# Performance work log

Measured on AMD Instinct MI355X. Metric: run time of the kernel, lower is better.

The kernel has to match this reference:

```python
import jax, jax.numpy as jnp
import numpy as np

N, K, DIM = 65536, 32, 64


def setup_inputs() -> dict:
    key = jax.random.key(0)
    k1, k2, k3, k4 = jax.random.split(key, 4)
    x = jax.random.normal(k1, (N, DIM), jnp.float32)
    log_pi = jax.random.normal(k2, (K, 1), jnp.float32)
    mu = jax.random.normal(k3, (K, DIM), jnp.float32)
    log_sigma_ = jax.random.normal(k4, (K, DIM, DIM), jnp.float32) / 100.0
    return {"x": x, "log_pi": log_pi, "mu": mu, "log_sigma_": log_sigma_}


def reference(x, log_pi, mu, log_sigma_):
    k, d = mu.shape
    # Faithful to torch: softmax over the size-1 last axis of (K,1) -> all ones.
    pi = jax.nn.softmax(log_pi, axis=-1)  # (K, 1)
    # scale_tril construction: strict lower triangle kept, diagonal -> exp(diag) + 1e-3
    diag = jnp.exp(jnp.diagonal(log_sigma_, axis1=-2, axis2=-1)) + 1e-3  # (K, d)
    L = jnp.tril(log_sigma_, -1) + jnp.eye(d, dtype=x.dtype) * diag[:, None, :]  # (K, d, d)
    # batched MVN log_prob via triangular solve
    diff = x[:, None, :] - mu[None, :, :]            # (N, K, d)
    b = jnp.transpose(diff, (1, 2, 0))               # (K, d, N)
    z = jax.scipy.linalg.solve_triangular(L, b, lower=True)  # (K, d, N)
    maha = jnp.sum(z * z, axis=1)                    # (K, N)
    logdet = jnp.sum(jnp.log(diag), axis=-1)         # (K,)
    logp = -0.5 * (maha + d * jnp.log(2.0 * jnp.pi)) - logdet[:, None]  # (K, N)
    p = jnp.exp(logp).T                              # (N, K)
    return jnp.log(jnp.matmul(p, pi).squeeze())      # (N,)
```

## Files before the change

### kernel.cpp

```cpp
#include <hip/hip_runtime.h>

#define KK 32
#define DD 64
#define NB 65536
#define PAD 68
#define FRAGS 6
#define SLOT (FRAGS * 64)
#define MREF 103.0f
#define L2E 1.4426950408889634f

typedef __attribute__((ext_vector_type(8))) short bf16x8;
typedef __attribute__((ext_vector_type(4))) float f32x4;
typedef __attribute__((ext_vector_type(16))) float f32x16;

__device__ inline short f2bf(float f) {
  uint32_t u = __builtin_bit_cast(uint32_t, f);
  uint32_t r = (u + 0x7fffu + ((u >> 16) & 1u)) >> 16;
  return (short)(r & 0xffffu);
}
__device__ inline uint4 pack8(const short* v) {
  uint4 u;
  u.x = (uint32_t)(unsigned short)v[0] | ((uint32_t)(unsigned short)v[1] << 16);
  u.y = (uint32_t)(unsigned short)v[2] | ((uint32_t)(unsigned short)v[3] << 16);
  u.z = (uint32_t)(unsigned short)v[4] | ((uint32_t)(unsigned short)v[5] << 16);
  u.w = (uint32_t)(unsigned short)v[6] | ((uint32_t)(unsigned short)v[7] << 16);
  return u;
}

__global__ __launch_bounds__(256) void md_prep(const float* __restrict__ ls,
                                               const float* __restrict__ mu,
                                               uint4* __restrict__ Bp,
                                               float* __restrict__ Cc,
                                               float* __restrict__ Kcl2) {
  __shared__ float Ls[DD * DD];
  __shared__ float Ys[DD * PAD];
  __shared__ float invdL[DD];
  __shared__ float muL[DD];
  const int k = blockIdx.x, t = threadIdx.x;
  const int j = t >> 2, sub = t & 3;
  const float* __restrict__ lsk = ls + (size_t)k * DD * DD;

#pragma unroll
  for (int it = 0; it < 4; ++it) {
    const int o = (it * 256 + t) * 4;
    *(float4*)&Ls[o] = *(const float4*)&lsk[o];
  }
  if (t < DD) muL[t] = mu[k * DD + t];
  __syncthreads();
  if (t < DD) invdL[t] = 1.0f / (expf(Ls[t * DD + t]) + 1e-3f);
  __syncthreads();

  const float invdj = invdL[j];
  float z[16];
#pragma unroll
  for (int mi = 0; mi < 16; ++mi) z[mi] = 0.f;
#pragma unroll
  for (int i = 0; i < DD; ++i) {
    float p = 0.f;
#pragma unroll
    for (int mi = 0; mi < 16; ++mi) {
      if (4 * mi < i) {
        const int m = 4 * mi + sub;
        p = fmaf(Ls[i * DD + m], (m < i) ? z[mi] : 0.f, p);
      }
    }
    p += __shfl_xor(p, 1, 64);
    p += __shfl_xor(p, 2, 64);
    const float zi = (i == j) ? invdj : -p * invdL[i];
    if (sub == (i & 3)) z[i >> 2] = zi;
  }
#pragma unroll
  for (int mi = 0; mi < 16; ++mi) Ys[(4 * mi + sub) * PAD + j] = z[mi];
  __syncthreads();

  {
    float p = 0.f;
#pragma unroll
    for (int mi = 0; mi < 16; ++mi) {
      const int m = 4 * mi + sub;
      p = fmaf(Ys[j * PAD + m], muL[m], p);
    }
    p += __shfl_xor(p, 1, 64);
    p += __shfl_xor(p, 2, 64);
    if (sub == 0) Cc[k * DD + j] = p;
  }

  if (t < DD) {
    float r = -logf(invdL[t]);
#pragma unroll
    for (int off = 32; off > 0; off >>= 1) r += __shfl_down(r, off, 64);
    if (t == 0)
      Kcl2[k] = (MREF - 0.5f * (64.0f * 1.83787706640934534f) - r) * L2E;
  }

  if (t < DD) {
    const int r32 = t & 31, h = t >> 5;
    uint4* slot = Bp + (size_t)k * SLOT;
#pragma unroll
    for (int it = 0; it < 2; ++it) {
#pragma unroll
      for (int kt = 0; kt < 4; ++kt) {
        if (it == 0 && kt >= 2) continue;
        const int i = it * 32 + r32;
        short hh[8];
#pragma unroll
        for (int jj = 0; jj < 8; ++jj) {
          const int m = kt * 16 + h * 8 + jj;
          const float v = Ys[i * PAD + m] - ((i == m) ? 1.0f : 0.0f);
          hh[jj] = f2bf(v);
        }
        const int fi = (it == 0) ? kt : (2 + kt);
        slot[fi * 64 + t] = pack8(hh);
      }
    }
  }
}

__global__ __launch_bounds__(256, 2) void md_main(const float* __restrict__ x,
                                                  const uint4* __restrict__ Bp,
                                                  const float* __restrict__ Cc,
                                                  const float* __restrict__ Kcl2,
                                                  float* __restrict__ out) {
  __shared__ float CcL[KK * DD];
  __shared__ float sOut[2 * 128];
  const int tid = threadIdx.x, lane = tid & 63, w = tid >> 6;
  const int sg = w & 1, kg = w >> 1;
  const int sblk = blockIdx.x;
  const int base = sblk * 128 + sg * 64;
  const int k0 = kg * 16;
  const int c32 = lane & 31, h = lane >> 5;

  bf16x8 Xb[2][4];
#pragma unroll
  for (int st = 0; st < 2; ++st) {
#pragma unroll
    for (int kt = 0; kt < 4; ++kt) {
      const float* src = x + (size_t)(base + st * 32 + c32) * DD + kt * 16 + h * 8;
      const float4 v0 = *(const float4*)src;
      const float4 v1 = *(const float4*)(src + 4);
      const float f[8] = {v0.x, v0.y, v0.z, v0.w, v1.x, v1.y, v1.z, v1.w};
      bf16x8 hb;
#pragma unroll
      for (int jj = 0; jj < 8; ++jj) hb[jj] = f2bf(f[jj]);
      Xb[st][kt] = hb;
    }
  }

  f32x16 xg[2][2];
#pragma unroll
  for (int it = 0; it < 2; ++it)
#pragma unroll
    for (int st = 0; st < 2; ++st)
#pragma unroll
      for (int g = 0; g < 4; ++g) {
        const f32x4 v = *(const f32x4*)&x[(size_t)(base + st * 32 + c32) * DD +
                                          it * 32 + g * 8 + 4 * h];
        xg[it][st][4 * g + 0] = v[0];
        xg[it][st][4 * g + 1] = v[1];
        xg[it][st][4 * g + 2] = v[2];
        xg[it][st][4 * g + 3] = v[3];
      }

#pragma unroll
  for (int it = 0; it < 8; ++it)
    CcL[it * 256 + tid] = Cc[it * 256 + tid];
  __syncthreads();

  float run_s[2] = {0.f, 0.f};

#pragma unroll
  for (int ci = 0; ci < 16; ++ci) {
    const int kabs = k0 + ci;
    const float kc = Kcl2[kabs];
    const uint4* __restrict__ buf = Bp + (size_t)kabs * SLOT;

    f32x4 cv[2][4];
#pragma unroll
    for (int it = 0; it < 2; ++it)
#pragma unroll
      for (int g = 0; g < 4; ++g)
        cv[it][g] = *(const f32x4*)&CcL[kabs * DD + it * 32 + g * 8 + 4 * h];

    const bf16x8 A0 = *(const bf16x8*)&buf[0 * 64 + lane];
    const bf16x8 A1 = *(const bf16x8*)&buf[1 * 64 + lane];
    const bf16x8 A2 = *(const bf16x8*)&buf[2 * 64 + lane];
    const bf16x8 A3 = *(const bf16x8*)&buf[3 * 64 + lane];
    const bf16x8 A4 = *(const bf16x8*)&buf[4 * 64 + lane];
    const bf16x8 A5 = *(const bf16x8*)&buf[5 * 64 + lane];

#pragma unroll
    for (int st = 0; st < 2; ++st) {
      f32x16 acc;
#pragma unroll
      for (int it = 0; it < 2; ++it) {
        f32x16 z;
#pragma unroll
        for (int g = 0; g < 4; ++g) {
#pragma unroll
          for (int r = 0; r < 4; ++r)
            z[4 * g + r] = xg[it][st][4 * g + r] - cv[it][g][r];
        }
        if (it == 0) {
          z = __builtin_amdgcn_mfma_f32_32x32x16_bf16(A0, Xb[st][0], z, 0, 0, 0);
          z = __builtin_amdgcn_mfma_f32_32x32x16_bf16(A1, Xb[st][1], z, 0, 0, 0);
          acc = z * z;
        } else {
          z = __builtin_amdgcn_mfma_f32_32x32x16_bf16(A2, Xb[st][0], z, 0, 0, 0);
          z = __builtin_amdgcn_mfma_f32_32x32x16_bf16(A3, Xb[st][1], z, 0, 0, 0);
          z = __builtin_amdgcn_mfma_f32_32x32x16_bf16(A4, Xb[st][2], z, 0, 0, 0);
          z = __builtin_amdgcn_mfma_f32_32x32x16_bf16(A5, Xb[st][3], z, 0, 0, 0);
          acc += z * z;
        }
      }
      const float t0 = (acc[0] + acc[1]) + (acc[2] + acc[3]);
      const float t1 = (acc[4] + acc[5]) + (acc[6] + acc[7]);
      const float t2 = (acc[8] + acc[9]) + (acc[10] + acc[11]);
      const float t3 = (acc[12] + acc[13]) + (acc[14] + acc[15]);
      float s = (t0 + t1) + (t2 + t3);
      s += __shfl_xor(s, 32, 64);
      const float tt = fmaf(-0.5f * L2E, s, kc);
      run_s[st] += __builtin_amdgcn_exp2f(tt);
    }
  }

  if (h == 0) {
#pragma unroll
    for (int st = 0; st < 2; ++st)
      sOut[kg * 128 + sg * 64 + st * 32 + c32] = run_s[st];
  }
  __syncthreads();
  if (tid < 128) {
    const float S = sOut[tid] + sOut[128 + tid];
    out[sblk * 128 + tid] = logf(S) - MREF;
  }
}

extern "C" void kernel_launch(void* const* d_in, const int* in_sizes, int n_in,
                              void* d_out, int out_size, void* d_ws, size_t ws_size,
                              hipStream_t stream) {
  const float* x  = (const float*)d_in[0];
  const float* mu = (const float*)d_in[2];
  const float* ls = (const float*)d_in[3];
  float* out = (float*)d_out;

  char* ws = (char*)d_ws;
  uint4* Bp   = (uint4*)ws;
  float* Cc   = (float*)(ws + (size_t)KK * SLOT * 16);
  float* Kcl2 = Cc + KK * DD;

  md_prep<<<KK, 256, 0, stream>>>(ls, mu, Bp, Cc, Kcl2);
  md_main<<<NB / 128, 256, 0, stream>>>(x, Bp, Cc, Kcl2, out);
}
```

Measured before the change: 98.33 us.

## Fuse prep and main kernels into one cooperative launch with grid sync

Merges the per-component precompute kernel and the main scoring kernel into a single cooperative kernel. The first 32 blocks run the prep work, every block loads its x fragments while prep runs, and a grid-wide sync separates the phases. This targets the second launch and the serialization gap between the two kernels, and overlaps the x loads with prep. It relies on all 512 blocks being co-resident, falls back to two launches if the cooperative launch fails, and adds the cost of a grid barrier plus the fused kernel's larger shared-memory footprint, which may reduce occupancy.

Result: slower. 167.7 us (+70.6%).

```diff
diff --git a/kernel.cpp b/kernel.cpp
--- a/kernel.cpp
+++ b/kernel.cpp
@@ -1,4 +1,7 @@
 #include <hip/hip_runtime.h>
+#include <hip/hip_cooperative_groups.h>
+
+namespace cg = cooperative_groups;
 
 #define KK 32
 #define DD 64
@@ -27,16 +30,14 @@
   return u;
 }
 
-__global__ __launch_bounds__(256) void md_prep(const float* __restrict__ ls,
-                                               const float* __restrict__ mu,
-                                               uint4* __restrict__ Bp,
-                                               float* __restrict__ Cc,
-                                               float* __restrict__ Kcl2) {
-  __shared__ float Ls[DD * DD];
-  __shared__ float Ys[DD * PAD];
-  __shared__ float invdL[DD];
-  __shared__ float muL[DD];
-  const int k = blockIdx.x, t = threadIdx.x;
+__device__ __forceinline__ void prep_body(int k, int t,
+                                          const float* __restrict__ ls,
+                                          const float* __restrict__ mu,
+                                          uint4* __restrict__ Bp,
+                                          float* __restrict__ Cc,
+                                          float* __restrict__ Kcl2,
+                                          float* Ls, float* Ys,
+                                          float* invdL, float* muL) {
   const int j = t >> 2, sub = t & 3;
   const float* __restrict__ lsk = ls + (size_t)k * DD * DD;
 
@@ -116,55 +117,17 @@
   }
 }
 
-__global__ __launch_bounds__(256, 2) void md_main(const float* __restrict__ x,
-                                                  const uint4* __restrict__ Bp,
-                                                  const float* __restrict__ Cc,
-                                                  const float* __restrict__ Kcl2,
-                                                  float* __restrict__ out) {
-  __shared__ float CcL[KK * DD];
-  __shared__ float sOut[2 * 128];
-  const int tid = threadIdx.x, lane = tid & 63, w = tid >> 6;
+__device__ __forceinline__ void main_tail(int tid, int sblk,
+                                          const bf16x8 Xb[2][4],
+                                          const f32x16 xg[2][2],
+                                          const uint4* __restrict__ Bp,
+                                          const float* __restrict__ Kcl2,
+                                          const float* CcL, float* sOut,
+                                          float* __restrict__ out) {
+  const int lane = tid & 63, w = tid >> 6;
   const int sg = w & 1, kg = w >> 1;
-  const int sblk = blockIdx.x;
-  const int base = sblk * 128 + sg * 64;
   const int k0 = kg * 16;
   const int c32 = lane & 31, h = lane >> 5;
-
-  bf16x8 Xb[2][4];
-#pragma unroll
-  for (int st = 0; st < 2; ++st) {
-#pragma unroll
-    for (int kt = 0; kt < 4; ++kt) {
-      const float* src = x + (size_t)(base + st * 32 + c32) * DD + kt * 16 + h * 8;
-      const float4 v0 = *(const float4*)src;
-      const float4 v1 = *(const float4*)(src + 4);
-      const float f[8] = {v0.x, v0.y, v0.z, v0.w, v1.x, v1.y, v1.z, v1.w};
-      bf16x8 hb;
-#pragma unroll
-      for (int jj = 0; jj < 8; ++jj) hb[jj] = f2bf(f[jj]);
-      Xb[st][kt] = hb;
-    }
-  }
-
-  f32x16 xg[2][2];
-#pragma unroll
-  for (int it = 0; it < 2; ++it)
-#pragma unroll
-    for (int st = 0; st < 2; ++st)
-#pragma unroll
-      for (int g = 0; g < 4; ++g) {
-        const f32x4 v = *(const f32x4*)&x[(size_t)(base + st * 32 + c32) * DD +
-                                          it * 32 + g * 8 + 4 * h];
-        xg[it][st][4 * g + 0] = v[0];
-        xg[it][st][4 * g + 1] = v[1];
-        xg[it][st][4 * g + 2] = v[2];
-        xg[it][st][4 * g + 3] = v[3];
-      }
-
-#pragma unroll
-  for (int it = 0; it < 8; ++it)
-    CcL[it * 256 + tid] = Cc[it * 256 + tid];
-  __syncthreads();
 
   float run_s[2] = {0.f, 0.f};
 
@@ -235,6 +198,109 @@
   }
 }
 
+__device__ __forceinline__ void load_x_frags(const float* __restrict__ x,
+                                             int base, int lane,
+                                             bf16x8 Xb[2][4], f32x16 xg[2][2]) {
+  const int c32 = lane & 31, h = lane >> 5;
+#pragma unroll
+  for (int st = 0; st < 2; ++st) {
+#pragma unroll
+    for (int kt = 0; kt < 4; ++kt) {
+      const float* src = x + (size_t)(base + st * 32 + c32) * DD + kt * 16 + h * 8;
+      const float4 v0 = *(const float4*)src;
+      const float4 v1 = *(const float4*)(src + 4);
+      const float f[8] = {v0.x, v0.y, v0.z, v0.w, v1.x, v1.y, v1.z, v1.w};
+      bf16x8 hb;
+#pragma unroll
+      for (int jj = 0; jj < 8; ++jj) hb[jj] = f2bf(f[jj]);
+      Xb[st][kt] = hb;
+    }
+  }
+#pragma unroll
+  for (int it = 0; it < 2; ++it)
+#pragma unroll
+    for (int st = 0; st < 2; ++st)
+#pragma unroll
+      for (int g = 0; g < 4; ++g) {
+        const f32x4 v = *(const f32x4*)&x[(size_t)(base + st * 32 + c32) * DD +
+                                          it * 32 + g * 8 + 4 * h];
+        xg[it][st][4 * g + 0] = v[0];
+        xg[it][st][4 * g + 1] = v[1];
+        xg[it][st][4 * g + 2] = v[2];
+        xg[it][st][4 * g + 3] = v[3];
+      }
+}
+
+__global__ __launch_bounds__(256, 2) void md_fused(const float* __restrict__ x,
+                                                   const float* __restrict__ ls,
+                                                   const float* __restrict__ mu,
+                                                   uint4* __restrict__ Bp,
+                                                   float* __restrict__ Cc,
+                                                   float* __restrict__ Kcl2,
+                                                   float* __restrict__ out) {
+  __shared__ float Ls[DD * DD];
+  __shared__ float Ys[DD * PAD];
+  __shared__ float invdL[DD];
+  __shared__ float muL[DD];
+  __shared__ float CcL[KK * DD];
+  __shared__ float sOut[2 * 128];
+  const int tid = threadIdx.x, lane = tid & 63, w = tid >> 6;
+  const int sblk = blockIdx.x;
+  const int base = sblk * 128 + (w & 1) * 64;
+
+  if (sblk < KK)
+    prep_body(sblk, tid, ls, mu, Bp, Cc, Kcl2, Ls, Ys, invdL, muL);
+
+  bf16x8 Xb[2][4];
+  f32x16 xg[2][2];
+  load_x_frags(x, base, lane, Xb, xg);
+
+  if (sblk < KK) __threadfence();
+  cg::this_grid().sync();
+
+#pragma unroll
+  for (int it = 0; it < 8; ++it)
+    CcL[it * 256 + tid] = Cc[it * 256 + tid];
+  __syncthreads();
+
+  main_tail(tid, sblk, Xb, xg, Bp, Kcl2, CcL, sOut, out);
+}
+
+__global__ __launch_bounds__(256) void md_prep(const float* __restrict__ ls,
+                                               const float* __restrict__ mu,
+                                               uint4* __restrict__ Bp,
+                                               float* __restrict__ Cc,
+                                               float* __restrict__ Kcl2) {
+  __shared__ float Ls[DD * DD];
+  __shared__ float Ys[DD * PAD];
+  __shared__ float invdL[DD];
+  __shared__ float muL[DD];
+  prep_body(blockIdx.x, threadIdx.x, ls, mu, Bp, Cc, Kcl2, Ls, Ys, invdL, muL);
+}
+
+__global__ __launch_bounds__(256, 2) void md_main(const float* __restrict__ x,
+                                                  const uint4* __restrict__ Bp,
+                                                  const float* __restrict__ Cc,
+                                                  const float* __restrict__ Kcl2,
+                                                  float* __restrict__ out) {
+  __shared__ float CcL[KK * DD];
+  __shared__ float sOut[2 * 128];
+  const int tid = threadIdx.x, lane = tid & 63, w = tid >> 6;
+  const int sblk = blockIdx.x;
+  const int base = sblk * 128 + (w & 1) * 64;
+
+  bf16x8 Xb[2][4];
+  f32x16 xg[2][2];
+  load_x_frags(x, base, lane, Xb, xg);
+
+#pragma unroll
+  for (int it = 0; it < 8; ++it)
+    CcL[it * 256 + tid] = Cc[it * 256 + tid];
+  __syncthreads();
+
+  main_tail(tid, sblk, Xb, xg, Bp, Kcl2, CcL, sOut, out);
+}
+
 extern "C" void kernel_launch(void* const* d_in, const int* in_sizes, int n_in,
                               void* d_out, int out_size, void* d_ws, size_t ws_size,
                               hipStream_t stream) {
@@ -248,6 +314,13 @@
   float* Cc   = (float*)(ws + (size_t)KK * SLOT * 16);
   float* Kcl2 = Cc + KK * DD;
 
-  md_prep<<<KK, 256, 0, stream>>>(ls, mu, Bp, Cc, Kcl2);
-  md_main<<<NB / 128, 256, 0, stream>>>(x, Bp, Cc, Kcl2, out);
-}
+  void* args[] = {(void*)&x, (void*)&ls, (void*)&mu, (void*)&Bp,
+                  (void*)&Cc, (void*)&Kcl2, (void*)&out};
+  hipError_t e = hipLaunchCooperativeKernel((const void*)md_fused,
+                                            dim3(NB / 128), dim3(256),
+                                            args, 0, stream);
+  if (e != hipSuccess) {
+    md_prep<<<KK, 256, 0, stream>>>(ls, mu, Bp, Cc, Kcl2);
+    md_main<<<NB / 128, 256, 0, stream>>>(x, Bp, Cc, Kcl2, out);
+  }
+}
```
